# Kernel tuning notes

Measured on AMD Instinct MI355X. Metric: run time of the kernel, lower is better.

The kernel has to match this reference:

```python
import jax, jax.numpy as jnp
import numpy as np

N = 1_500_000  # nodes (250k tracklets x 6 hits)
E = 12_000_000  # edges


def setup_inputs() -> dict:
    key = jax.random.key(0)
    ks = jax.random.split(key, 26)
    w = lambda k, shape: (jax.random.normal(k, shape, jnp.float32) * 0.1)
    inp = {
        "x": jax.random.normal(ks[0], (N, 1), jnp.float32),
        "edge_index": jax.random.randint(ks[1], (2, E), 0, N),
        "edge_attr": jax.random.normal(ks[2], (E, 2), jnp.float32),
        # conv1: in=1, prop=9, edge=2, out=9
        "Wx1": w(ks[3], (9, 1)), "bx1": w(ks[4], (9,)),
        "We1": w(ks[5], (9, 2)), "be1": w(ks[6], (9,)),
        "Wo1": w(ks[7], (9, 9)), "bo1": w(ks[8], (9,)),
        # conv2: in=9, prop=9, edge=2, out=9
        "Wx2": w(ks[9], (9, 9)), "bx2": w(ks[10], (9,)),
        "We2": w(ks[11], (9, 2)), "be2": w(ks[12], (9,)),
        "Wo2": w(ks[13], (9, 9)), "bo2": w(ks[14], (9,)),
        # conv3: in=9, prop=9, edge=2, out=4
        "Wx3": w(ks[15], (9, 9)), "bx3": w(ks[16], (9,)),
        "We3": w(ks[17], (9, 2)), "be3": w(ks[18], (9,)),
        "Wo3": w(ks[19], (4, 9)), "bo3": w(ks[20], (4,)),
        # head MLP
        "W1": w(ks[21], (8, 24)), "b1": w(ks[22], (8,)),
        "W2": w(ks[23], (4, 8)), "b2": w(ks[24], (4,)),
    }
    return inp


def _conv(x, src, dst, edge_attr, Wx, bx, We, be, Wo, bo):
    # trackletGNN: lin_x -> gather x_j -> * lin_edge(edge_attr) -> scatter-add -> lin_out
    h = x @ Wx.T + bx                      # [N, P]
    msg = h[src] * (edge_attr @ We.T + be)  # [E, P] gather + edge linear + multiply
    agg = jax.ops.segment_sum(msg, dst, num_segments=x.shape[0])  # [N, P]
    return agg @ Wo.T + bo


def reference(x, edge_index, edge_attr,
              Wx1, bx1, We1, be1, Wo1, bo1,
              Wx2, bx2, We2, be2, Wo2, bo2,
              Wx3, bx3, We3, be3, Wo3, bo3,
              W1, b1, W2, b2):
    src, dst = edge_index[0], edge_index[1]
    h = jax.nn.relu(_conv(x, src, dst, edge_attr, Wx1, bx1, We1, be1, Wo1, bo1))
    h = jax.nn.relu(_conv(h, src, dst, edge_attr, Wx2, bx2, We2, be2, Wo2, bo2))
    h = jax.nn.relu(_conv(h, src, dst, edge_attr, Wx3, bx3, We3, be3, Wo3, bo3))
    h = h.reshape(-1, 24)                   # 6 nodes x 4 feats per tracklet
    h = jax.nn.relu(h @ W1.T + b1)
    h = h @ W2.T + b2
    return jax.nn.log_softmax(h, axis=1)
```

## Files before the change

kernel.cpp:

```cpp
#include <hip/hip_runtime.h>
#include <hip/hip_bf16.h>


#define NNODES 1500000
#define NEDGES 12000000
#define NTRACK 250000
#define BSH    9
#define BSZ    512
#define BMASK  511u
#define NBUCK  2930
#define PCHUNK 4096
#define PBLK   2930
#define HCHUNK 32768
#define HBLK   367
#define SRCMASK 0x1FFFFFu
#define NSLICE 48
#define SRTR   20
#define FXSCALE 16777216.f
#define FXINV   (1.f / 16777216.f)

typedef unsigned int   u32;
typedef unsigned short u16;

static __device__ __forceinline__ float b2f(u32 v) {
    union { float f; u32 u; } x; x.u = v << 16; return x.f;
}
static __device__ __forceinline__ u16 f2b(float f) {
    __hip_bfloat16 h = __float2bfloat16(f);
    return *reinterpret_cast<u16*>(&h);
}
static __device__ __forceinline__ float ldw(const void* p, int i, int isf32) {
    return isf32 ? ((const float*)p)[i] : b2f((u32)((const u16*)p)[i]);
}
static __device__ __forceinline__ int fx(float f) {
    return (int)rintf(f * FXSCALE);
}


__global__ void k_detect(const u16* a, const u16* b, const u16* c,
                         const u16* d, const u16* e, const u16* f,
                         int* flag) {
    if (blockIdx.x == 0 && threadIdx.x == 0) {
        int isf32 = 0;
        const u16* ps[6] = {a, b, c, d, e, f};
        const int  ns[6] = {9, 9, 9, 9, 9, 8};
        for (int k = 0; k < 6; k++)
            for (int i = 0; i < ns[k]; i++) {
                float v = b2f((u32)ps[k][i]);
                if (!(fabsf(v) < 1.0e3f)) isf32 = 1;
            }
        *flag = isf32;
    }
}


__global__ __launch_bounds__(256) void k_xcast(const void* __restrict__ x,
                                               u16* __restrict__ xb,
                                               const int* __restrict__ flag) {
    int isf32 = *flag;
    int n = blockIdx.x * 256 + threadIdx.x;
    if (n < NNODES)
        xb[n] = isf32 ? f2b(((const float*)x)[n]) : ((const u16*)x)[n];
}


__global__ __launch_bounds__(512) void k_bhist(const int* __restrict__ dst,
                                               int* __restrict__ gh) {
    __shared__ u32 h[NBUCK];
    int t = threadIdx.x;
    for (int b = t; b < NBUCK; b += 512) h[b] = 0;
    __syncthreads();
    int c0 = blockIdx.x * HCHUNK;
#pragma unroll 4
    for (int i = 0; i < HCHUNK / 512; i++) {
        int e = c0 + i * 512 + t;
        if (e < NEDGES) atomicAdd(&h[((u32)dst[e]) >> BSH], 1u);
    }
    __syncthreads();
    for (int b = t; b < NBUCK; b += 512) {
        u32 c = h[b];
        if (c) atomicAdd((u32*)&gh[b], c);
    }
}

__global__ __launch_bounds__(256) void k_bscan(const int* __restrict__ gh,
                                               int* __restrict__ bstart,
                                               int* __restrict__ gcur) {
    __shared__ u32 sd[256];
    __shared__ u32 carry;
    int t = threadIdx.x;
    if (t == 0) carry = 0;
    __syncthreads();
    for (int c0 = 0; c0 < NBUCK; c0 += 256) {
        int b = c0 + t;
        u32 v = (b < NBUCK) ? (u32)gh[b] : 0;
        sd[t] = v; __syncthreads();
        for (int o = 1; o < 256; o <<= 1) {
            u32 a = (t >= o) ? sd[t - o] : 0;
            __syncthreads();
            sd[t] += a;
            __syncthreads();
        }
        u32 excl = carry + sd[t] - v;
        if (b < NBUCK) { bstart[b] = (int)excl; gcur[b] = (int)excl; }
        __syncthreads();
        if (t == 255) carry += sd[255];
        __syncthreads();
    }
    if (t == 0) bstart[NBUCK] = NEDGES;
}


__global__ __launch_bounds__(512) void k_part(const int* __restrict__ src,
                                              const int* __restrict__ dst,
                                              const void* __restrict__ attr,
                                              int* __restrict__ gcur,
                                              uint2* __restrict__ perm,
                                              const int* __restrict__ flag) {
    __shared__ int   cur[NBUCK];
    __shared__ int   gbA[NBUCK];
    __shared__ uint2 rec[PCHUNK];
    __shared__ u32   sd[512];
    __shared__ u32   carryS;
    int isf32 = *flag;
    int t = threadIdx.x;
    int c0 = blockIdx.x * PCHUNK;
    int chunkN = NEDGES - c0; if (chunkN > PCHUNK) chunkN = PCHUNK;

    for (int b = t; b < NBUCK; b += 512) cur[b] = 0;
    if (t == 0) carryS = 0;
    __syncthreads();

    int ds_[8], sr_[8];
#pragma unroll
    for (int k = 0; k < 8; k++) {
        int e = c0 + k * 512 + t;
        if (e < NEDGES) {
            ds_[k] = dst[e];
            sr_[k] = src[e];
            atomicAdd((u32*)&cur[((u32)ds_[k]) >> BSH], 1u);
        } else { ds_[k] = -1; sr_[k] = 0; }
    }
    __syncthreads();

    for (int b0 = 0; b0 < NBUCK; b0 += 512) {
        int b = b0 + t;
        u32 v = (b < NBUCK) ? (u32)cur[b] : 0;
        sd[t] = v; __syncthreads();
        for (int o = 1; o < 512; o <<= 1) {
            u32 a = (t >= o) ? sd[t - o] : 0;
            __syncthreads();
            sd[t] += a;
            __syncthreads();
        }
        u32 excl = carryS + sd[t] - v;
        if (b < NBUCK) {
            cur[b] = (int)excl;
            if (v) gbA[b] = atomicAdd(&gcur[b], (int)v) - (int)excl;
        }
        __syncthreads();
        if (t == 511) carryS += sd[511];
        __syncthreads();
    }

#pragma unroll
    for (int k = 0; k < 8; k++) {
        int e = c0 + k * 512 + t;
        if (e < NEDGES) {
            u32 d  = (u32)ds_[k];
            u32 fb = d >> BSH;
            u32 ap;
            if (isf32) {
                float2 a = ((const float2*)attr)[e];
                ap = (u32)f2b(a.x) | ((u32)f2b(a.y) << 16);
            } else {
                ap = ((const u32*)attr)[e];
            }
            int slot = atomicAdd(&cur[fb], 1);
            uint2 r; r.x = ((u32)sr_[k]) | ((d & BMASK) << 21); r.y = ap;
            rec[slot] = r;
        }
    }
    __syncthreads();

#pragma unroll
    for (int j = 0; j < 8; j++) {
        int s = j * 512 + t;
        if (s < chunkN) {
            int lo = 0, hi = NBUCK - 1;
            while (lo < hi) {
                int mid = (lo + hi) >> 1;
                if (cur[mid] > s) hi = mid; else lo = mid + 1;
            }
            perm[gbA[lo] + s] = rec[s];
        }
    }
}


__global__ __launch_bounds__(256) void k_srt(const int* __restrict__ bstart,
                                             uint2* __restrict__ perm) {
    __shared__ int h[NSLICE];
    int t = threadIdx.x;
    int b = blockIdx.x;
    int r0 = bstart[b], r1 = bstart[b + 1];
    int len = r1 - r0;
    if (len <= 0) return;
    if (len > SRTR * 256) return;
    if (t < NSLICE) h[t] = 0;
    __syncthreads();

    uint2 r[SRTR];
#pragma unroll
    for (int k = 0; k < SRTR; k++) {
        int i = r0 + k * 256 + t;
        if (i < r1) {
            r[k] = perm[i];
            atomicAdd(&h[(r[k].x & SRCMASK) >> 15], 1);
        } else {
            r[k].x = 0xFFFFFFFFu;
        }
    }
    __syncthreads();

    if (t == 0) {
        int s = 0;
        for (int k = 0; k < NSLICE; k++) { int c = h[k]; h[k] = s; s += c; }
    }
    __syncthreads();

#pragma unroll
    for (int k = 0; k < SRTR; k++) {
        if (r[k].x != 0xFFFFFFFFu) {
            int slot = atomicAdd(&h[(r[k].x & SRCMASK) >> 15], 1);
            perm[r0 + slot] = r[k];
        }
    }
}


__global__ __launch_bounds__(256) void k_eagg1(
        const int* __restrict__ bstart, const uint2* __restrict__ perm,
        const u16* __restrict__ xb,
        const void* Wx, const void* bx, const void* We, const void* be,
        const void* Wo, const void* bo, const void* Wxn, const void* bxn,
        uint4* __restrict__ hA, u16* __restrict__ hB,
        const int* __restrict__ flag) {
    __shared__ int acc[BSZ * 9];
    __shared__ float sWx[9], sbx[9], sWe[18], sbe[9], sWo[81], sbo[9], sWxn[81], sbxn[9];
    int isf32 = *flag;
    int t = threadIdx.x;
    if (t < 9)  sWx[t]  = ldw(Wx,  t, isf32);
    if (t < 9)  sbx[t]  = ldw(bx,  t, isf32);
    if (t < 18) sWe[t]  = ldw(We,  t, isf32);
    if (t < 9)  sbe[t]  = ldw(be,  t, isf32);
    if (t < 81) sWo[t]  = ldw(Wo,  t, isf32);
    if (t < 9)  sbo[t]  = ldw(bo,  t, isf32);
    if (t < 81) sWxn[t] = ldw(Wxn, t, isf32);
    if (t < 9)  sbxn[t] = ldw(bxn, t, isf32);
    for (int i = t; i < BSZ * 9; i += 256) acc[i] = 0;
    __syncthreads();

    int b = blockIdx.x;
    int r0 = bstart[b], r1 = bstart[b + 1];
    for (int i = r0 + t; i < r1; i += 256) {
        uint2 rec = perm[i];
        int   l   = (int)((rec.x >> 21) & BMASK);
        float xs  = b2f((u32)xb[rec.x & SRCMASK]);
        float a0  = b2f(rec.y & 0xffffu);
        float a1  = b2f(rec.y >> 16);
        int* ap = &acc[l * 9];
#pragma unroll
        for (int j = 0; j < 9; j++) {
            float e  = fmaf(a0, sWe[2 * j], fmaf(a1, sWe[2 * j + 1], sbe[j]));
            float hh = fmaf(xs, sWx[j], sbx[j]);
            atomicAdd(&ap[j], fx(hh * e));
        }
    }
    __syncthreads();

    for (int l = t; l < BSZ; l += 256) {
        int n = b * BSZ + l;
        if (n >= NNODES) break;
        float av[9];
#pragma unroll
        for (int j = 0; j < 9; j++) av[j] = (float)acc[l * 9 + j] * FXINV;
        float o[9];
#pragma unroll
        for (int k = 0; k < 9; k++) {
            float v = sbo[k];
#pragma unroll
            for (int j = 0; j < 9; j++) v = fmaf(av[j], sWo[k * 9 + j], v);
            o[k] = fmaxf(v, 0.f);
        }
        u16 hv[9];
#pragma unroll
        for (int j = 0; j < 9; j++) {
            float v = sbxn[j];
#pragma unroll
            for (int k = 0; k < 9; k++) v = fmaf(o[k], sWxn[j * 9 + k], v);
            hv[j] = f2b(v);
        }
        uint4 q;
        q.x = (u32)hv[0] | ((u32)hv[1] << 16);
        q.y = (u32)hv[2] | ((u32)hv[3] << 16);
        q.z = (u32)hv[4] | ((u32)hv[5] << 16);
        q.w = (u32)hv[6] | ((u32)hv[7] << 16);
        hA[n] = q;
        hB[n] = hv[8];
    }
}


template <int OUTF, bool FUSE_NEXT>
__global__ __launch_bounds__(256) void k_eagg(
        const int* __restrict__ bstart, const uint2* __restrict__ perm,
        const uint4* __restrict__ hA, const u16* __restrict__ hB,
        const void* We, const void* be, const void* Wo, const void* bo,
        const void* Wxn, const void* bxn,
        uint4* __restrict__ oA, u16* __restrict__ oB,
        const int* __restrict__ flag) {
    __shared__ int acc[BSZ * 9];
    __shared__ float sWe[18], sbe[9], sWo[OUTF * 9], sbo[OUTF];
    __shared__ float sWxn[FUSE_NEXT ? 81 : 1], sbxn[FUSE_NEXT ? 9 : 1];
    int isf32 = *flag;
    int t = threadIdx.x;
    if (t < 18)       sWe[t] = ldw(We, t, isf32);
    if (t < 9)        sbe[t] = ldw(be, t, isf32);
    if (t < OUTF * 9) sWo[t] = ldw(Wo, t, isf32);
    if (t < OUTF)     sbo[t] = ldw(bo, t, isf32);
    if constexpr (FUSE_NEXT) {
        if (t < 81) sWxn[t] = ldw(Wxn, t, isf32);
        if (t < 9)  sbxn[t] = ldw(bxn, t, isf32);
    }
    for (int i = t; i < BSZ * 9; i += 256) acc[i] = 0;
    __syncthreads();

    int b = blockIdx.x;
    int r0 = bstart[b], r1 = bstart[b + 1];
    for (int i = r0 + t; i < r1; i += 256) {
        uint2 rec = perm[i];
        int   s   = (int)(rec.x & SRCMASK);
        int   l   = (int)((rec.x >> 21) & BMASK);
        float a0  = b2f(rec.y & 0xffffu);
        float a1  = b2f(rec.y >> 16);
        uint4 qa  = hA[s];
        u32   qb  = (u32)hB[s];
        float ev[9];
#pragma unroll
        for (int j = 0; j < 9; j++)
            ev[j] = fmaf(a0, sWe[2 * j], fmaf(a1, sWe[2 * j + 1], sbe[j]));
        float h[9];
        h[0] = b2f(qa.x & 0xffffu); h[1] = b2f(qa.x >> 16);
        h[2] = b2f(qa.y & 0xffffu); h[3] = b2f(qa.y >> 16);
        h[4] = b2f(qa.z & 0xffffu); h[5] = b2f(qa.z >> 16);
        h[6] = b2f(qa.w & 0xffffu); h[7] = b2f(qa.w >> 16);
        h[8] = b2f(qb);
        int* ap = &acc[l * 9];
#pragma unroll
        for (int j = 0; j < 9; j++)
            atomicAdd(&ap[j], fx(h[j] * ev[j]));
    }
    __syncthreads();

    for (int l = t; l < BSZ; l += 256) {
        int n = b * BSZ + l;
        if (n >= NNODES) break;
        float av[9];
#pragma unroll
        for (int j = 0; j < 9; j++) av[j] = (float)acc[l * 9 + j] * FXINV;
        float o[OUTF];
#pragma unroll
        for (int k = 0; k < OUTF; k++) {
            float v = sbo[k];
#pragma unroll
            for (int j = 0; j < 9; j++) v = fmaf(av[j], sWo[k * 9 + j], v);
            o[k] = fmaxf(v, 0.f);
        }
        if constexpr (FUSE_NEXT) {
            u16 hv[9];
#pragma unroll
            for (int j = 0; j < 9; j++) {
                float v = sbxn[j];
#pragma unroll
                for (int k = 0; k < OUTF; k++) v = fmaf(o[k], sWxn[j * 9 + k], v);
                hv[j] = f2b(v);
            }
            uint4 q;
            q.x = (u32)hv[0] | ((u32)hv[1] << 16);
            q.y = (u32)hv[2] | ((u32)hv[3] << 16);
            q.z = (u32)hv[4] | ((u32)hv[5] << 16);
            q.w = (u32)hv[6] | ((u32)hv[7] << 16);
            oA[n] = q;
            oB[n] = hv[8];
        } else {
            uint2 q;
            q.x = (u32)f2b(o[0]) | ((u32)f2b(o[1]) << 16);
            q.y = (u32)f2b(o[2]) | ((u32)f2b(o[3]) << 16);
            ((uint2*)oA)[n] = q;
        }
    }
}


__global__ __launch_bounds__(256) void k_head(
        const u16* __restrict__ f,
        const void* W1, const void* b1, const void* W2, const void* b2,
        void* __restrict__ out, const int* __restrict__ flag) {
    __shared__ float sW1[192], sb1[8], sW2[32], sb2[4];
    int isf32 = *flag;
    int t = threadIdx.x;
    if (t < 192) sW1[t] = ldw(W1, t, isf32);
    if (t < 8)   sb1[t] = ldw(b1, t, isf32);
    if (t < 32)  sW2[t] = ldw(W2, t, isf32);
    if (t < 4)   sb2[t] = ldw(b2, t, isf32);
    __syncthreads();

    int tr = blockIdx.x * 256 + t;
    if (tr >= NTRACK) return;

    const uint4* fp = (const uint4*)(f + (size_t)tr * 24);
    uint4 A = fp[0], B = fp[1], C = fp[2];
    u32 w[12] = {A.x, A.y, A.z, A.w, B.x, B.y, B.z, B.w, C.x, C.y, C.z, C.w};
    float in[24];
#pragma unroll
    for (int i = 0; i < 12; i++) {
        in[2 * i]     = b2f(w[i] & 0xffffu);
        in[2 * i + 1] = b2f(w[i] >> 16);
    }

    float z1[8];
#pragma unroll
    for (int o = 0; o < 8; o++) {
        float v = sb1[o];
#pragma unroll
        for (int i = 0; i < 24; i++) v = fmaf(in[i], sW1[o * 24 + i], v);
        z1[o] = fmaxf(v, 0.f);
    }
    float z2[4];
#pragma unroll
    for (int c = 0; c < 4; c++) {
        float v = sb2[c];
#pragma unroll
        for (int o = 0; o < 8; o++) v = fmaf(z1[o], sW2[c * 8 + o], v);
        z2[c] = v;
    }
    float m = fmaxf(fmaxf(z2[0], z2[1]), fmaxf(z2[2], z2[3]));
    float s = 0.f;
#pragma unroll
    for (int c = 0; c < 4; c++) s += expf(z2[c] - m);
    float l = logf(s) + m;

    if (isf32) {
        float4 q; q.x = z2[0] - l; q.y = z2[1] - l; q.z = z2[2] - l; q.w = z2[3] - l;
        ((float4*)((float*)out + (size_t)tr * 4))[0] = q;
    } else {
        uint2 q;
        q.x = (u32)f2b(z2[0] - l) | ((u32)f2b(z2[1] - l) << 16);
        q.y = (u32)f2b(z2[2] - l) | ((u32)f2b(z2[3] - l) << 16);
        ((uint2*)((u16*)out + (size_t)tr * 4))[0] = q;
    }
}


extern "C" void kernel_launch(void* const* d_in, const int* in_sizes, int n_in,
                              void* d_out, int out_size, void* d_ws, size_t ws_size,
                              hipStream_t stream) {
    const void* X    = d_in[0];
    const int* eidx  = (const int*)d_in[1];
    const void* eattr= d_in[2];
    const void *WX1 = d_in[3],  *BX1 = d_in[4];
    const void *WE1 = d_in[5],  *BE1 = d_in[6];
    const void *WO1 = d_in[7],  *BO1 = d_in[8];
    const void *WX2 = d_in[9],  *BX2 = d_in[10];
    const void *WE2 = d_in[11], *BE2 = d_in[12];
    const void *WO2 = d_in[13], *BO2 = d_in[14];
    const void *WX3 = d_in[15], *BX3 = d_in[16];
    const void *WE3 = d_in[17], *BE3 = d_in[18];
    const void *WO3 = d_in[19], *BO3 = d_in[20];
    const void *W1  = d_in[21], *B1  = d_in[22];
    const void *W2  = d_in[23], *B2  = d_in[24];

    const int* src = eidx;
    const int* dst = eidx + NEDGES;

    char* w = (char*)d_ws;
    size_t off = 0;
    auto take = [&](size_t bytes) -> void* {
        void* p = w + off;
        off += (bytes + 255) & ~(size_t)255;
        return p;
    };
    int*   flag   = (int*)take(256);
    int*   gh     = (int*)take((size_t)NBUCK * 4);
    int*   bstart = (int*)take((size_t)(NBUCK + 1) * 4);
    int*   gcur   = (int*)take((size_t)NBUCK * 4);
    u16*   xb     = (u16*)take((size_t)NNODES * 2);
    uint2* perm   = (uint2*)take((size_t)NEDGES * 8);
    uint4* hA2    = (uint4*)take((size_t)NNODES * 16);
    u16*   hB2    = (u16*)take((size_t)NNODES * 2);
    uint4* hA3    = (uint4*)take((size_t)NNODES * 16);
    u16*   hB3    = (u16*)take((size_t)NNODES * 2);
    u16*   f      = (u16*)hA2;
    (void)ws_size; (void)n_in; (void)in_sizes; (void)out_size;

    const int NB = (NNODES + 255) / 256;
    const int TB = (NTRACK + 255) / 256;

    hipMemsetAsync(gh, 0, (size_t)NBUCK * 4, stream);

    k_detect <<<1,    64,  0, stream>>>((const u16*)BX1, (const u16*)BE1, (const u16*)BO1,
                                        (const u16*)BX2, (const u16*)BE2, (const u16*)B1, flag);
    k_xcast  <<<NB,   256, 0, stream>>>(X, xb, flag);
    k_bhist  <<<HBLK, 512, 0, stream>>>(dst, gh);
    k_bscan  <<<1,    256, 0, stream>>>(gh, bstart, gcur);
    k_part   <<<PBLK, 512, 0, stream>>>(src, dst, eattr, gcur, perm, flag);
    k_srt    <<<NBUCK,256, 0, stream>>>(bstart, perm);

    k_eagg1        <<<NBUCK, 256, 0, stream>>>(bstart, perm, xb,
                                               WX1, BX1, WE1, BE1, WO1, BO1, WX2, BX2,
                                               hA2, hB2, flag);
    k_eagg<9,true> <<<NBUCK, 256, 0, stream>>>(bstart, perm, hA2, hB2,
                                               WE2, BE2, WO2, BO2, WX3, BX3,
                                               hA3, hB3, flag);
    k_eagg<4,false><<<NBUCK, 256, 0, stream>>>(bstart, perm, hA3, hB3,
                                               WE3, BE3, WO3, BO3, WO3, BO3,
                                               (uint4*)f, (u16*)f, flag);
    k_head         <<<TB,    256, 0, stream>>>(f, W1, B1, W2, B2, d_out, flag);
}
```

Measured before the change: 1.044 ms.

## Make edge bucket partition deterministic with per-chunk histograms and matrix scan

Replaces the global-atomic bucket cursor with a per-chunk histogram matrix, a two-level column scan (per segment, then across segments), and precomputed per-chunk global offsets, so each partition block knows its output positions without atomics on global memory. The partition kernel also records each slot's bucket id in shared memory, which removes the binary search over bucket starts during scatter. The cost is an extra pass over dst, about 17MB of count and offset matrices to write and read, and two more kernel launches.

```diff
diff --git a/kernel.cpp b/kernel.cpp
--- a/kernel.cpp
+++ b/kernel.cpp
@@ -11,8 +11,9 @@
 #define NBUCK  2930
 #define PCHUNK 4096
 #define PBLK   2930
-#define HCHUNK 32768
-#define HBLK   367
+#define NSEG   8
+#define SEGC   367
+#define NTILE  46
 #define SRCMASK 0x1FFFFFu
 #define NSLICE 48
 #define SRTR   20
@@ -64,28 +65,49 @@
 }
 
 
-__global__ __launch_bounds__(512) void k_bhist(const int* __restrict__ dst,
-                                               int* __restrict__ gh) {
+__global__ __launch_bounds__(512) void k_hist(const int* __restrict__ dst,
+                                              u16* __restrict__ cnt) {
     __shared__ u32 h[NBUCK];
     int t = threadIdx.x;
+    int chunk = blockIdx.x;
+    int c0 = chunk * PCHUNK;
     for (int b = t; b < NBUCK; b += 512) h[b] = 0;
     __syncthreads();
-    int c0 = blockIdx.x * HCHUNK;
+#pragma unroll
+    for (int k = 0; k < 8; k++) {
+        int e = c0 + k * 512 + t;
+        if (e < NEDGES) atomicAdd(&h[((u32)dst[e]) >> BSH], 1u);
+    }
+    __syncthreads();
+    size_t row = (size_t)chunk * NBUCK;
+    for (int b = t; b < NBUCK; b += 512) cnt[row + b] = (u16)h[b];
+}
+
+
+__global__ __launch_bounds__(64) void k_mscanA(const u16* __restrict__ cnt,
+                                               u16* __restrict__ offm,
+                                               u16* __restrict__ st) {
+    int seg  = blockIdx.x / NTILE;
+    int tile = blockIdx.x % NTILE;
+    int b = tile * 64 + threadIdx.x;
+    if (b >= NBUCK) return;
+    int cS = seg * SEGC;
+    int cE = cS + SEGC; if (cE > PBLK) cE = PBLK;
+    u32 run = 0;
 #pragma unroll 4
-    for (int i = 0; i < HCHUNK / 512; i++) {
-        int e = c0 + i * 512 + t;
-        if (e < NEDGES) atomicAdd(&h[((u32)dst[e]) >> BSH], 1u);
-    }
-    __syncthreads();
-    for (int b = t; b < NBUCK; b += 512) {
-        u32 c = h[b];
-        if (c) atomicAdd((u32*)&gh[b], c);
-    }
-}
-
-__global__ __launch_bounds__(256) void k_bscan(const int* __restrict__ gh,
-                                               int* __restrict__ bstart,
-                                               int* __restrict__ gcur) {
+    for (int c = cS; c < cE; c++) {
+        size_t idx = (size_t)c * NBUCK + b;
+        u32 v = (u32)cnt[idx];
+        offm[idx] = (u16)run;
+        run += v;
+    }
+    st[(size_t)seg * NBUCK + b] = (u16)run;
+}
+
+
+__global__ __launch_bounds__(256) void k_mscanB(const u16* __restrict__ st,
+                                                int* __restrict__ bstart,
+                                                u32* __restrict__ segb) {
     __shared__ u32 sd[256];
     __shared__ u32 carry;
     int t = threadIdx.x;
@@ -93,16 +115,27 @@
     __syncthreads();
     for (int c0 = 0; c0 < NBUCK; c0 += 256) {
         int b = c0 + t;
-        u32 v = (b < NBUCK) ? (u32)gh[b] : 0;
-        sd[t] = v; __syncthreads();
+        u32 tot = 0;
+        if (b < NBUCK)
+#pragma unroll
+            for (int s = 0; s < NSEG; s++) tot += (u32)st[(size_t)s * NBUCK + b];
+        sd[t] = tot; __syncthreads();
         for (int o = 1; o < 256; o <<= 1) {
             u32 a = (t >= o) ? sd[t - o] : 0;
             __syncthreads();
             sd[t] += a;
             __syncthreads();
         }
-        u32 excl = carry + sd[t] - v;
-        if (b < NBUCK) { bstart[b] = (int)excl; gcur[b] = (int)excl; }
+        u32 excl = carry + sd[t] - tot;
+        if (b < NBUCK) {
+            bstart[b] = (int)excl;
+            u32 r = excl;
+#pragma unroll
+            for (int s = 0; s < NSEG; s++) {
+                segb[(size_t)s * NBUCK + b] = r;
+                r += (u32)st[(size_t)s * NBUCK + b];
+            }
+        }
         __syncthreads();
         if (t == 255) carry += sd[255];
         __syncthreads();
@@ -114,38 +147,32 @@
 __global__ __launch_bounds__(512) void k_part(const int* __restrict__ src,
                                               const int* __restrict__ dst,
                                               const void* __restrict__ attr,
-                                              int* __restrict__ gcur,
+                                              const u16* __restrict__ cnt,
+                                              const u16* __restrict__ offm,
+                                              const u32* __restrict__ segb,
                                               uint2* __restrict__ perm,
                                               const int* __restrict__ flag) {
-    __shared__ int   cur[NBUCK];
-    __shared__ int   gbA[NBUCK];
+    __shared__ u32   cur[NBUCK];
+    __shared__ u32   gbA[NBUCK];
     __shared__ uint2 rec[PCHUNK];
-    __shared__ u32   sd[512];
+    __shared__ u16   bid[PCHUNK];
     __shared__ u32   carryS;
+    u32* sd = reinterpret_cast<u32*>(rec);
     int isf32 = *flag;
     int t = threadIdx.x;
-    int c0 = blockIdx.x * PCHUNK;
+    int chunk = blockIdx.x;
+    int seg = chunk / SEGC;
+    int c0 = chunk * PCHUNK;
     int chunkN = NEDGES - c0; if (chunkN > PCHUNK) chunkN = PCHUNK;
-
-    for (int b = t; b < NBUCK; b += 512) cur[b] = 0;
+    size_t row = (size_t)chunk * NBUCK;
+
+    for (int b = t; b < NBUCK; b += 512) cur[b] = (u32)cnt[row + b];
     if (t == 0) carryS = 0;
-    __syncthreads();
-
-    int ds_[8], sr_[8];
-#pragma unroll
-    for (int k = 0; k < 8; k++) {
-        int e = c0 + k * 512 + t;
-        if (e < NEDGES) {
-            ds_[k] = dst[e];
-            sr_[k] = src[e];
-            atomicAdd((u32*)&cur[((u32)ds_[k]) >> BSH], 1u);
-        } else { ds_[k] = -1; sr_[k] = 0; }
-    }
     __syncthreads();
 
     for (int b0 = 0; b0 < NBUCK; b0 += 512) {
         int b = b0 + t;
-        u32 v = (b < NBUCK) ? (u32)cur[b] : 0;
+        u32 v = (b < NBUCK) ? cur[b] : 0;
         sd[t] = v; __syncthreads();
         for (int o = 1; o < 512; o <<= 1) {
             u32 a = (t >= o) ? sd[t - o] : 0;
@@ -154,20 +181,22 @@
             __syncthreads();
         }
         u32 excl = carryS + sd[t] - v;
-        if (b < NBUCK) {
-            cur[b] = (int)excl;
-            if (v) gbA[b] = atomicAdd(&gcur[b], (int)v) - (int)excl;
-        }
+        if (b < NBUCK) cur[b] = excl;
         __syncthreads();
         if (t == 511) carryS += sd[511];
         __syncthreads();
     }
 
+    for (int b = t; b < NBUCK; b += 512)
+        gbA[b] = segb[(size_t)seg * NBUCK + b] + (u32)offm[row + b] - cur[b];
+    __syncthreads();
+
 #pragma unroll
     for (int k = 0; k < 8; k++) {
         int e = c0 + k * 512 + t;
         if (e < NEDGES) {
-            u32 d  = (u32)ds_[k];
+            u32 d = (u32)dst[e];
+            u32 s = (u32)src[e];
             u32 fb = d >> BSH;
             u32 ap;
             if (isf32) {
@@ -176,9 +205,10 @@
             } else {
                 ap = ((const u32*)attr)[e];
             }
-            int slot = atomicAdd(&cur[fb], 1);
-            uint2 r; r.x = ((u32)sr_[k]) | ((d & BMASK) << 21); r.y = ap;
+            int slot = (int)atomicAdd(&cur[fb], 1u);
+            uint2 r; r.x = s | ((d & BMASK) << 21); r.y = ap;
             rec[slot] = r;
+            bid[slot] = (u16)fb;
         }
     }
     __syncthreads();
@@ -187,12 +217,8 @@
     for (int j = 0; j < 8; j++) {
         int s = j * 512 + t;
         if (s < chunkN) {
-            int lo = 0, hi = NBUCK - 1;
-            while (lo < hi) {
-                int mid = (lo + hi) >> 1;
-                if (cur[mid] > s) hi = mid; else lo = mid + 1;
-            }
-            perm[gbA[lo] + s] = rec[s];
+            u32 fb = (u32)bid[s];
+            perm[gbA[fb] + s] = rec[s];
         }
     }
 }
@@ -492,9 +518,11 @@
         return p;
     };
     int*   flag   = (int*)take(256);
-    int*   gh     = (int*)take((size_t)NBUCK * 4);
     int*   bstart = (int*)take((size_t)(NBUCK + 1) * 4);
-    int*   gcur   = (int*)take((size_t)NBUCK * 4);
+    u16*   cnt    = (u16*)take((size_t)PBLK * NBUCK * 2);
+    u16*   offm   = (u16*)take((size_t)PBLK * NBUCK * 2);
+    u16*   st     = (u16*)take((size_t)NSEG * NBUCK * 2);
+    u32*   segb   = (u32*)take((size_t)NSEG * NBUCK * 4);
     u16*   xb     = (u16*)take((size_t)NNODES * 2);
     uint2* perm   = (uint2*)take((size_t)NEDGES * 8);
     uint4* hA2    = (uint4*)take((size_t)NNODES * 16);
@@ -507,14 +535,13 @@
     const int NB = (NNODES + 255) / 256;
     const int TB = (NTRACK + 255) / 256;
 
-    hipMemsetAsync(gh, 0, (size_t)NBUCK * 4, stream);
-
     k_detect <<<1,    64,  0, stream>>>((const u16*)BX1, (const u16*)BE1, (const u16*)BO1,
                                         (const u16*)BX2, (const u16*)BE2, (const u16*)B1, flag);
     k_xcast  <<<NB,   256, 0, stream>>>(X, xb, flag);
-    k_bhist  <<<HBLK, 512, 0, stream>>>(dst, gh);
-    k_bscan  <<<1,    256, 0, stream>>>(gh, bstart, gcur);
-    k_part   <<<PBLK, 512, 0, stream>>>(src, dst, eattr, gcur, perm, flag);
+    k_hist   <<<PBLK, 512, 0, stream>>>(dst, cnt);
+    k_mscanA <<<NSEG * NTILE, 64, 0, stream>>>(cnt, offm, st);
+    k_mscanB <<<1,    256, 0, stream>>>(st, bstart, segb);
+    k_part   <<<PBLK, 512, 0, stream>>>(src, dst, eattr, cnt, offm, segb, perm, flag);
     k_srt    <<<NBUCK,256, 0, stream>>>(bstart, perm);
 
     k_eagg1        <<<NBUCK, 256, 0, stream>>>(bstart, perm, xb,
```

Result: no change. 1.042 ms (-0.2%).
